# Kernel tuning notes

Measured on AMD Instinct MI355X. Metric: run time of the kernel, lower is better.

The kernel has to match this reference:

```python
import jax, jax.numpy as jnp
import numpy as np

D, L, C, CP, H, HD, QB, KB = 8, 2048, 128, 16, 4, 32, 32, 128
NQ = L // QB

def _ln(x, eps=1e-5):
    m = jnp.mean(x, axis=-1, keepdims=True)
    v = jnp.var(x, axis=-1, keepdims=True)
    return (x - m) * jax.lax.rsqrt(v + eps)

def _ada_ln(a, s, Wg, bg, Ws):
    # AF3 AdaLN: gated layernorm conditioned on s
    an = _ln(a); sn = _ln(s)
    return jax.nn.sigmoid(sn @ Wg + bg) * an + sn @ Ws

def setup_inputs() -> dict:
    key = jax.random.key(0)
    ks = jax.random.split(key, 32)
    p = lambda i, shape: jax.random.normal(ks[i], shape, dtype=jnp.float32) * 0.02
    inp = {}
    inp['A_I'] = jax.random.normal(ks[0], (D, L, C), dtype=jnp.float32)
    inp['S_I'] = jax.random.normal(ks[1], (D, L, C), dtype=jnp.float32)
    inp['Z_II'] = jax.random.normal(ks[2], (1, L, L, CP), dtype=jnp.float32)
    # static sliding-window indices: 128-key window centered on each 32-query block
    inp['indicesQ'] = jnp.arange(L, dtype=jnp.int64).reshape(NQ, QB)
    kraw = (jnp.arange(NQ) * QB - (KB - QB) // 2)[:, None] + jnp.arange(KB)[None, :]
    inp['indicesK'] = jnp.clip(kraw, 0, L - 1).astype(jnp.int64)
    inp['maskQ_float'] = jnp.zeros((NQ, QB), jnp.float32)
    inp['maskK_float'] = ((kraw < 0) | (kraw >= L)).astype(jnp.float32)
    # parameters
    inp['ada1_Wg'] = p(3, (C, C)); inp['ada1_bg'] = jnp.zeros((C,), jnp.float32); inp['ada1_Ws'] = p(4, (C, C))
    inp['Wq'] = p(5, (C, H * HD)); inp['bq'] = jnp.zeros((H * HD,), jnp.float32)
    inp['Wk'] = p(6, (C, H * HD)); inp['Wv'] = p(7, (C, H * HD))
    inp['ln0_g'] = jnp.ones((CP,), jnp.float32); inp['ln0_b'] = jnp.zeros((CP,), jnp.float32)
    inp['Wb'] = p(8, (CP, H))
    inp['Wg_attn'] = p(9, (C, H * HD))
    inp['Wa'] = p(10, (H * HD, C))
    inp['Wop'] = p(11, (C, C)); inp['bop'] = jnp.full((C,), -2.0, jnp.float32)
    inp['ada2_Wg'] = p(12, (C, C)); inp['ada2_bg'] = jnp.zeros((C,), jnp.float32); inp['ada2_Ws'] = p(13, (C, C))
    inp['W_sw'] = p(14, (C, 2 * C)); inp['W_lin'] = p(15, (C, 2 * C))
    inp['ct_Wg'] = p(16, (C, C)); inp['ct_bg'] = jnp.full((C,), -2.0, jnp.float32)
    inp['W_out2'] = p(17, (2 * C, C))
    return inp

def _forward(A_I, S_I, Z_II, indicesQ, indicesK, maskQ_float, maskK_float,
             ada1_Wg, ada1_bg, ada1_Ws, Wq, bq, Wk, Wv, ln0_g, ln0_b, Wb,
             Wg_attn, Wa, Wop, bop, ada2_Wg, ada2_bg, ada2_Ws, W_sw, W_lin,
             ct_Wg, ct_bg, W_out2):
    Dn, Lv = A_I.shape[0], A_I.shape[1]
    An = _ada_ln(A_I, S_I, ada1_Wg, ada1_bg, ada1_Ws)
    Q = (An @ Wq + bq).reshape(Dn, Lv, H, HD)
    K = (An @ Wk).reshape(Dn, Lv, H, HD)
    V = (An @ Wv).reshape(Dn, Lv, H, HD)
    B = ((_ln(Z_II) * ln0_g + ln0_b) @ Wb)[0]        # [L, L, H]
    G = jax.nn.sigmoid(An @ Wg_attn).reshape(Dn, Lv, H, HD)
    qs = Q[:, indicesQ]                              # [D, nq, qb, H, hd]
    ksub = K[:, indicesK]                            # [D, nq, kb, H, hd]
    vs = V[:, indicesK]
    attn = jnp.einsum('dnihc,dnjhc->dnijh', qs, ksub) / jnp.sqrt(jnp.float32(HD))
    bias = B[indicesQ[:, :, None], indicesK[:, None, :]]  # [nq, qb, kb, H]
    attn = attn + bias[None]
    mask = maskQ_float[None, :, :, None, None] + maskK_float[None, :, None, :, None]
    attn = attn - 1e9 * mask
    attn = jax.nn.softmax(attn, axis=-2)             # softmax over key window (j)
    af = jnp.einsum('dnijh,dnjhc->dnihc', attn, vs)
    af = af * (1.0 - maskQ_float)[None, :, :, None, None]
    af = af.reshape(Dn, -1, H, HD)[:, :Lv]
    af = (G * af).reshape(Dn, Lv, H * HD) @ Wa
    B_I = jax.nn.sigmoid(S_I @ Wop + bop) * af
    A = A_I + B_I
    an2 = _ada_ln(A, S_I, ada2_Wg, ada2_bg, ada2_Ws)
    b = jax.nn.silu(an2 @ W_sw) * (an2 @ W_lin)      # SwiGLU transition
    A = A + jax.nn.sigmoid(S_I @ ct_Wg + ct_bg) * (b @ W_out2)
    return A

def reference(A_I, S_I, Z_II, indicesQ, indicesK, maskQ_float, maskK_float,
              ada1_Wg, ada1_bg, ada1_Ws, Wq, bq, Wk, Wv, ln0_g, ln0_b, Wb,
              Wg_attn, Wa, Wop, bop, ada2_Wg, ada2_bg, ada2_Ws, W_sw, W_lin,
              ct_Wg, ct_bg, W_out2):
    return _forward(A_I, S_I, Z_II, indicesQ, indicesK, maskQ_float, maskK_float,
                    ada1_Wg, ada1_bg, ada1_Ws, Wq, bq, Wk, Wv, ln0_g, ln0_b, Wb,
                    Wg_attn, Wa, Wop, bop, ada2_Wg, ada2_bg, ada2_Ws, W_sw, W_lin,
                    ct_Wg, ct_bg, W_out2)
```

## Files before the change

kernel.cpp:

```cpp
#include <hip/hip_runtime.h>

#define DL 16384
#define LL 2048
#define NQB 64
#define QBS 32
#define KBS 128

typedef __attribute__((ext_vector_type(8))) short short8;
typedef __attribute__((ext_vector_type(4))) short short4v;
typedef __attribute__((ext_vector_type(4))) float f32x4;

__device__ __forceinline__ float sigmoidf_(float x) { return 1.f / (1.f + expf(-x)); }

__device__ __forceinline__ short f2bf(float f) {
    union { float f; unsigned u; } v; v.f = f;
    unsigned r = (v.u + 0x7FFFu + ((v.u >> 16) & 1u)) >> 16;
    return (short)r;
}
__device__ __forceinline__ float bf2f(short h) {
    union { unsigned u; float f; } v; v.u = ((unsigned)(unsigned short)h) << 16;
    return v.f;
}
__device__ __forceinline__ unsigned packbf16(short a, short b) {
    return ((unsigned)(unsigned short)a) | (((unsigned)(unsigned short)b) << 16);
}

#define AFRAG(buf, stride, r0, kk) (*(const short8*)&(buf)[(size_t)((r0) + cl) * (stride) + (kk) * 32 + kg * 8])
#define WFRAG(Wt, K, n0, kk) (*(const short8*)((Wt) + (size_t)((n0) + cl) * (K) + (kk) * 32 + kg * 8))
#define MFMA(acc, a, b) acc = __builtin_amdgcn_mfma_f32_16x16x32_bf16(a, b, acc, 0, 0, 0)

__global__ __launch_bounds__(256) void k_wtrans(
    const float* __restrict__ W0, const float* __restrict__ W1, const float* __restrict__ W2,
    const float* __restrict__ W3, const float* __restrict__ W4, const float* __restrict__ W5,
    const float* __restrict__ W6, const float* __restrict__ W7, const float* __restrict__ W8,
    const float* __restrict__ W9, const float* __restrict__ W10,
    const float* __restrict__ Wsw, const float* __restrict__ Wlin, const float* __restrict__ Wout2,
    short* __restrict__ wout)
{
    __shared__ float sW[128 * 128];
    const int b = blockIdx.x;
    const int tid = threadIdx.x;
    const float* srcs[14] = {W0,W1,W2,W3,W4,W5,W6,W7,W8,W9,W10,Wsw,Wlin,Wout2};
    const int sel[17]  = {0,1,2,3,4,5,6,7,8,9,10,11,11,12,12,13,13};
    const int soff[17] = {0,0,0,0,0,0,0,0,0,0,0, 0,128, 0,128, 0,16384};
    const int sN[17]   = {128,128,128,128,128,128,128,128,128,128,128, 256,256,256,256, 128,128};
    const int doff[17] = {0,16384,32768,49152,65536,81920,98304,114688,131072,147456,163840,
                          180224,196608, 212992,229376, 245760,245888};
    const int dK[17]   = {128,128,128,128,128,128,128,128,128,128,128, 128,128,128,128, 256,256};
    const float* src = srcs[sel[b]] + soff[b];
    const int srcN = sN[b];
    short* dst = wout + doff[b];
    const int dstK = dK[b];
    {
        const int r = tid >> 1, ch = (tid & 1) * 64;
        #pragma unroll
        for (int u = 0; u < 16; ++u) {
            float4 v = *(const float4*)(src + (size_t)r * srcN + ch + u * 4);
            *(float4*)&sW[r * 128 + ch + u * 4] = v;
        }
    }
    __syncthreads();
    {
        const int o = tid >> 1, kh = (tid & 1) * 64;
        #pragma unroll
        for (int u8 = 0; u8 < 8; ++u8) {
            short8 pk;
            #pragma unroll
            for (int e = 0; e < 8; ++e)
                pk[e] = f2bf(sW[(kh + u8 * 8 + e) * 128 + o]);
            *(short8*)(dst + (size_t)o * dstK + kh + u8 * 8) = pk;
        }
    }
}

__global__ __launch_bounds__(512) void k_main(
    const float* __restrict__ A_I, const float* __restrict__ S_I,
    const short* __restrict__ Wg1t, const short* __restrict__ Ws1t,
    const short* __restrict__ Wqt, const short* __restrict__ Wkt,
    const short* __restrict__ Wvt, const short* __restrict__ Wgat,
    const float* __restrict__ bg1, const float* __restrict__ bq,
    const float* __restrict__ Z, const float* __restrict__ g16, const float* __restrict__ b16,
    const float* __restrict__ Wb,
    short* __restrict__ Qo, short* __restrict__ Ko, short* __restrict__ Vo, short* __restrict__ Go,
    short* __restrict__ BBt)
{
    __shared__ short sAr[32 * 136];
    __shared__ short sSn[32 * 136];
    __shared__ short sAn[32 * 136];
    __shared__ float sMean[32], sRstd[32];
    __shared__ float sWb[64], sg[16], sb[16];
    __shared__ short sT[4 * 4 * 128];
    const int bid = blockIdx.x;
    const int tid = threadIdx.x;
    const int lane = tid & 63;

    if (bid >= 512) {
        const int bb = bid - 512;
        const int n = bb >> 3;
        const int io = (bb & 7) * 4;
        if (tid < 64) sWb[tid] = Wb[tid];
        if (tid < 16) { sg[tid] = g16[tid]; sb[tid] = b16[tid]; }
        __syncthreads();
        {
            int il = tid >> 7, j = tid & 127;
            int i = io + il;
            int kr = n * 32 - 48 + j;
            int kc = min(max(kr, 0), LL - 1);
            const float4* z4 = (const float4*)(Z + ((long)(n * 32 + i) * LL + kc) * 16);
            float zv[16];
            #pragma unroll
            for (int w = 0; w < 4; ++w) {
                float4 v = z4[w];
                zv[w * 4 + 0] = v.x; zv[w * 4 + 1] = v.y; zv[w * 4 + 2] = v.z; zv[w * 4 + 3] = v.w;
            }
            float sm = 0.f, sq = 0.f;
            #pragma unroll
            for (int cp = 0; cp < 16; ++cp) { sm += zv[cp]; sq = fmaf(zv[cp], zv[cp], sq); }
            float m = sm * (1.f / 16.f);
            float rs = rsqrtf(sq * (1.f / 16.f) - m * m + 1e-5f);
            float b0 = 0.f, b1 = 0.f, b2 = 0.f, b3 = 0.f;
            #pragma unroll
            for (int cp = 0; cp < 16; ++cp) {
                float zn = (zv[cp] - m) * rs * sg[cp] + sb[cp];
                b0 = fmaf(zn, sWb[cp * 4 + 0], b0);
                b1 = fmaf(zn, sWb[cp * 4 + 1], b1);
                b2 = fmaf(zn, sWb[cp * 4 + 2], b2);
                b3 = fmaf(zn, sWb[cp * 4 + 3], b3);
            }
            sT[(0 * 4 + il) * 128 + j] = f2bf(b0);
            sT[(1 * 4 + il) * 128 + j] = f2bf(b1);
            sT[(2 * 4 + il) * 128 + j] = f2bf(b2);
            sT[(3 * 4 + il) * 128 + j] = f2bf(b3);
        }
        __syncthreads();
        {
            int hh = tid >> 7, rem = tid & 127;
            int il = rem >> 5, jb = (rem & 31) * 4;
            short4v pk = *(const short4v*)&sT[(hh * 4 + il) * 128 + jb];
            *(short4v*)(BBt + (((size_t)n * 4 + hh) * 32 + io + il) * 128 + jb) = pk;
        }
        return;
    }

    const long t0 = (long)bid * 32;
    {
        const int row = tid >> 4, seg = tid & 15;
        const float* ap = A_I + (t0 + row) * 128 + seg * 8;
        const float* sp = S_I + (t0 + row) * 128 + seg * 8;
        float av[8], sv[8];
        #pragma unroll
        for (int u = 0; u < 2; ++u) {
            float4 a4 = ((const float4*)ap)[u];
            float4 s4 = ((const float4*)sp)[u];
            av[4*u] = a4.x; av[4*u+1] = a4.y; av[4*u+2] = a4.z; av[4*u+3] = a4.w;
            sv[4*u] = s4.x; sv[4*u+1] = s4.y; sv[4*u+2] = s4.z; sv[4*u+3] = s4.w;
        }
        float am = 0.f, aq = 0.f, sm = 0.f, sq = 0.f;
        #pragma unroll
        for (int u = 0; u < 8; ++u) {
            am += av[u]; aq = fmaf(av[u], av[u], aq);
            sm += sv[u]; sq = fmaf(sv[u], sv[u], sq);
        }
        am += __shfl_xor(am, 1); am += __shfl_xor(am, 2); am += __shfl_xor(am, 4); am += __shfl_xor(am, 8);
        aq += __shfl_xor(aq, 1); aq += __shfl_xor(aq, 2); aq += __shfl_xor(aq, 4); aq += __shfl_xor(aq, 8);
        sm += __shfl_xor(sm, 1); sm += __shfl_xor(sm, 2); sm += __shfl_xor(sm, 4); sm += __shfl_xor(sm, 8);
        sq += __shfl_xor(sq, 1); sq += __shfl_xor(sq, 2); sq += __shfl_xor(sq, 4); sq += __shfl_xor(sq, 8);
        float amean = am * (1.f / 128.f);
        float arstd = rsqrtf(aq * (1.f / 128.f) - amean * amean + 1e-5f);
        float smean = sm * (1.f / 128.f);
        float srstd = rsqrtf(sq * (1.f / 128.f) - smean * smean + 1e-5f);
        if ((tid & 15) == 0) { sMean[row] = amean; sRstd[row] = arstd; }
        short8 pa, ps;
        #pragma unroll
        for (int e = 0; e < 8; ++e) {
            pa[e] = f2bf(av[e]);
            ps[e] = f2bf((sv[e] - smean) * srstd);
        }
        *(short8*)&sAr[row * 136 + seg * 8] = pa;
        *(short8*)&sSn[row * 136 + seg * 8] = ps;
    }
    __syncthreads();
    const int w = tid >> 6;
    const int n0 = w * 16;
    const int cl = lane & 15, kg = lane >> 4;
    {
        short8 wg[4], wsf[4];
        #pragma unroll
        for (int kk = 0; kk < 4; ++kk) {
            wg[kk]  = WFRAG(Wg1t, 128, n0, kk);
            wsf[kk] = WFRAG(Ws1t, 128, n0, kk);
        }
        #pragma unroll
        for (int mt = 0; mt < 2; ++mt) {
            f32x4 ag = {0.f, 0.f, 0.f, 0.f}, as = {0.f, 0.f, 0.f, 0.f};
            #pragma unroll
            for (int kk = 0; kk < 4; ++kk) {
                short8 a = AFRAG(sSn, 136, mt * 16, kk);
                MFMA(ag, wg[kk], a);
                MFMA(as, wsf[kk], a);
            }
            const int tok = mt * 16 + cl;
            const int c0 = n0 + kg * 4;
            float4 bg4 = *(const float4*)&bg1[c0];
            float mean = sMean[tok], rstd = sRstd[tok];
            short4v ar4 = *(const short4v*)&sAr[tok * 136 + c0];
            short4v o;
            #pragma unroll
            for (int i = 0; i < 4; ++i) {
                float an = (bf2f(ar4[i]) - mean) * rstd;
                float An = sigmoidf_(ag[i] + ((const float*)&bg4)[i]) * an + as[i];
                o[i] = f2bf(An);
            }
            *(short4v*)&sAn[tok * 136 + c0] = o;
        }
    }
    __syncthreads();
    {
        const float SCL = 0.17677669529663687f;
        short8 af[2][4];
        #pragma unroll
        for (int mt = 0; mt < 2; ++mt)
            #pragma unroll
            for (int kk = 0; kk < 4; ++kk)
                af[mt][kk] = AFRAG(sAn, 136, mt * 16, kk);
        const int c0 = n0 + kg * 4;
        float4 bq4 = *(const float4*)&bq[c0];
        #pragma unroll
        for (int m = 0; m < 4; ++m) {
            const short* Wt = (m == 0) ? Wqt : (m == 1) ? Wkt : (m == 2) ? Wvt : Wgat;
            short8 wf[4];
            #pragma unroll
            for (int kk = 0; kk < 4; ++kk) wf[kk] = WFRAG(Wt, 128, n0, kk);
            #pragma unroll
            for (int mt = 0; mt < 2; ++mt) {
                f32x4 acc = {0.f, 0.f, 0.f, 0.f};
                #pragma unroll
                for (int kk = 0; kk < 4; ++kk) MFMA(acc, wf[kk], af[mt][kk]);
                long t = t0 + mt * 16 + cl;
                short4v o;
                if (m == 0) {
                    #pragma unroll
                    for (int i = 0; i < 4; ++i) o[i] = f2bf((acc[i] + ((const float*)&bq4)[i]) * SCL);
                    *(short4v*)(Qo + t * 128 + c0) = o;
                } else if (m == 1) {
                    #pragma unroll
                    for (int i = 0; i < 4; ++i) o[i] = f2bf(acc[i]);
                    *(short4v*)(Ko + t * 128 + c0) = o;
                } else if (m == 2) {
                    #pragma unroll
                    for (int i = 0; i < 4; ++i) o[i] = f2bf(acc[i]);
                    *(short4v*)(Vo + t * 128 + c0) = o;
                } else {
                    #pragma unroll
                    for (int i = 0; i < 4; ++i) o[i] = f2bf(sigmoidf_(acc[i]));
                    *(short4v*)(Go + t * 128 + c0) = o;
                }
            }
        }
    }
}

__global__ __launch_bounds__(512) void k_attn_postf(
    const short* __restrict__ Qg, const short* __restrict__ Kg, const short* __restrict__ Vg,
    const short* __restrict__ Gg, const short* __restrict__ BBt, const float* __restrict__ maskK,
    const float* __restrict__ S_I, const float* __restrict__ A_I,
    const short* __restrict__ Wat, const short* __restrict__ Wopt, const short* __restrict__ ctWgt,
    const short* __restrict__ Wg2t, const short* __restrict__ Ws2t,
    const short* __restrict__ Wswt, const short* __restrict__ Wlint, const short* __restrict__ Wout2t,
    const float* __restrict__ bop, const float* __restrict__ ctbg, const float* __restrict__ bg2,
    float* __restrict__ Out)
{
    __shared__ __align__(16) char smem[78336];
    short* sAF  = (short*)smem;
    short* vts  = (short*)(smem + 8704);
    short* Pl   = (short*)(smem + 43520);
    short* sS   = (short*)(smem + 8704);
    short* sSn  = (short*)(smem + 17408);
    float* sA   = (float*)(smem + 26112);
    float* sMean = (float*)(smem + 43008);
    float* sRstd = (float*)(smem + 43136);
    short* sAn2 = sAF;
    short* sB   = (short*)(smem + 8704);

    const int n = blockIdx.x, d = blockIdx.y;
    const int tid = threadIdx.x;
    const int lane = tid & 63;
    const long tb = (long)d * LL;
    const long t0 = tb + n * 32;
    const int kbase = n * 32 - 48;
    const int cl = lane & 15, kg = lane >> 4;
    const int w = tid >> 6;
    const int h = w >> 1, amt = w & 1;

    {
        const int unit = tid >> 1, half = tid & 1;
        const int hh = unit >> 6, j0 = (unit & 63) * 2;
        int kc0 = min(max(kbase + j0, 0), LL - 1);
        int kc1 = min(max(kbase + j0 + 1, 0), LL - 1);
        const short8* p0 = (const short8*)(Vg + (tb + kc0) * 128 + hh * 32 + half * 16);
        const short8* p1 = (const short8*)(Vg + (tb + kc1) * 128 + hh * 32 + half * 16);
        short8 e0 = p0[0], e1 = p0[1];
        short8 o0 = p1[0], o1 = p1[1];
        short* vh = vts + hh * 4352;
        #pragma unroll
        for (int e = 0; e < 8; ++e)
            *(unsigned*)&vh[(half * 16 + e) * 136 + j0] = packbf16(e0[e], o0[e]);
        #pragma unroll
        for (int e = 0; e < 8; ++e)
            *(unsigned*)&vh[(half * 16 + 8 + e) * 136 + j0] = packbf16(e1[e], o1[e]);
    }

    float sc[8][4];
    {
        short8 qf = *(const short8*)(Qg + (t0 + amt * 16 + cl) * 128 + h * 32 + kg * 8);
        #pragma unroll
        for (int nt = 0; nt < 8; ++nt) {
            int kc = min(max(kbase + nt * 16 + cl, 0), LL - 1);
            short8 kf = *(const short8*)(Kg + (tb + kc) * 128 + h * 32 + kg * 8);
            f32x4 s = {0.f, 0.f, 0.f, 0.f};
            MFMA(s, kf, qf);
            float4 mk4 = *(const float4*)(maskK + n * 128 + nt * 16 + kg * 4);
            short4v bfr = *(const short4v*)(BBt + (((size_t)n * 4 + h) * 32 + amt * 16 + cl) * 128 + nt * 16 + kg * 4);
            #pragma unroll
            for (int i = 0; i < 4; ++i)
                sc[nt][i] = s[i] + bf2f(bfr[i]) - ((const float*)&mk4)[i] * 1e9f;
        }
    }
    {
        float mx = sc[0][0];
        #pragma unroll
        for (int nt = 0; nt < 8; ++nt)
            #pragma unroll
            for (int i = 0; i < 4; ++i) mx = fmaxf(mx, sc[nt][i]);
        mx = fmaxf(mx, __shfl_xor(mx, 16));
        mx = fmaxf(mx, __shfl_xor(mx, 32));
        float sm = 0.f;
        #pragma unroll
        for (int nt = 0; nt < 8; ++nt)
            #pragma unroll
            for (int i = 0; i < 4; ++i) {
                float p = __expf(sc[nt][i] - mx);
                sc[nt][i] = p; sm += p;
            }
        sm += __shfl_xor(sm, 16);
        sm += __shfl_xor(sm, 32);
        float inv = 1.f / sm;
        short* PH = Pl + h * 4352;
        const int tok = amt * 16 + cl;
        #pragma unroll
        for (int nt = 0; nt < 8; ++nt) {
            short4v p4;
            #pragma unroll
            for (int i = 0; i < 4; ++i) p4[i] = f2bf(sc[nt][i] * inv);
            *(short4v*)&PH[tok * 136 + nt * 16 + kg * 4] = p4;
        }
    }

    const int prow = tid >> 4, pseg = tid & 15;
    float pav[8], psv[8];
    {
        const float* apI = A_I + (t0 + prow) * 128 + pseg * 8;
        const float* spI = S_I + (t0 + prow) * 128 + pseg * 8;
        #pragma unroll
        for (int u = 0; u < 2; ++u) {
            float4 a4 = ((const float4*)apI)[u];
            float4 s4 = ((const float4*)spI)[u];
            pav[4*u] = a4.x; pav[4*u+1] = a4.y; pav[4*u+2] = a4.z; pav[4*u+3] = a4.w;
            psv[4*u] = s4.x; psv[4*u+1] = s4.y; psv[4*u+2] = s4.z; psv[4*u+3] = s4.w;
        }
    }

    __syncthreads();
    {
        short* PH = Pl + h * 4352;
        short* vh = vts + h * 4352;
        const int tok = amt * 16 + cl;
        short8 pfr[4];
        #pragma unroll
        for (int kk = 0; kk < 4; ++kk)
            pfr[kk] = *(const short8*)&PH[tok * 136 + kk * 32 + kg * 8];
        #pragma unroll
        for (int ct = 0; ct < 2; ++ct) {
            f32x4 acc = {0.f, 0.f, 0.f, 0.f};
            #pragma unroll
            for (int kk = 0; kk < 4; ++kk) {
                short8 a = *(const short8*)&vh[(ct * 16 + cl) * 136 + kk * 32 + kg * 8];
                MFMA(acc, a, pfr[kk]);
            }
            const int c0 = h * 32 + ct * 16 + kg * 4;
            short4v g4 = *(const short4v*)(Gg + (t0 + tok) * 128 + c0);
            short4v o4;
            #pragma unroll
            for (int i = 0; i < 4; ++i) o4[i] = f2bf(bf2f(g4[i]) * acc[i]);
            *(short4v*)&sAF[tok * 136 + c0] = o4;
        }
    }
    __syncthreads();

    {
        #pragma unroll
        for (int u = 0; u < 2; ++u)
            *(float4*)&sA[prow * 132 + pseg * 8 + u * 4] = *(const float4*)&pav[u * 4];
        float sm = 0.f, sq = 0.f;
        #pragma unroll
        for (int u = 0; u < 8; ++u) { sm += psv[u]; sq = fmaf(psv[u], psv[u], sq); }
        sm += __shfl_xor(sm, 1); sm += __shfl_xor(sm, 2); sm += __shfl_xor(sm, 4); sm += __shfl_xor(sm, 8);
        sq += __shfl_xor(sq, 1); sq += __shfl_xor(sq, 2); sq += __shfl_xor(sq, 4); sq += __shfl_xor(sq, 8);
        float smean = sm * (1.f / 128.f);
        float srstd = rsqrtf(sq * (1.f / 128.f) - smean * smean + 1e-5f);
        short8 pr, pn;
        #pragma unroll
        for (int e = 0; e < 8; ++e) {
            float s = psv[e];
            pr[e] = f2bf(s);
            pn[e] = f2bf((s - smean) * srstd);
        }
        *(short8*)&sS [prow * 136 + pseg * 8] = pr;
        *(short8*)&sSn[prow * 136 + pseg * 8] = pn;
    }
    __syncthreads();
    const int n0 = w * 16;
    const int c0 = n0 + kg * 4;
    float g2s[8];

    {
        short8 wA[4], wO[4], wG[4];
        #pragma unroll
        for (int kk = 0; kk < 4; ++kk) {
            wA[kk] = WFRAG(Wat, 128, n0, kk);
            wO[kk] = WFRAG(Wopt, 128, n0, kk);
            wG[kk] = WFRAG(ctWgt, 128, n0, kk);
        }
        float4 bop4 = *(const float4*)&bop[c0];
        float4 ct4  = *(const float4*)&ctbg[c0];
        #pragma unroll
        for (int rt = 0; rt < 2; ++rt) {
            f32x4 aA = {0.f,0.f,0.f,0.f}, aO = {0.f,0.f,0.f,0.f}, aG = {0.f,0.f,0.f,0.f};
            #pragma unroll
            for (int kk = 0; kk < 4; ++kk) {
                short8 af = AFRAG(sAF, 136, rt * 16, kk);
                short8 sf = AFRAG(sS, 136, rt * 16, kk);
                MFMA(aA, wA[kk], af);
                MFMA(aO, wO[kk], sf);
                MFMA(aG, wG[kk], sf);
            }
            const int tok = rt * 16 + cl;
            float4 Av = *(const float4*)&sA[tok * 132 + c0];
            float4 outv;
            #pragma unroll
            for (int i = 0; i < 4; ++i) {
                ((float*)&outv)[i] = ((const float*)&Av)[i]
                    + sigmoidf_(aO[i] + ((const float*)&bop4)[i]) * aA[i];
                g2s[rt * 4 + i] = sigmoidf_(aG[i] + ((const float*)&ct4)[i]);
            }
            *(float4*)&sA[tok * 132 + c0] = outv;
        }
    }
    __syncthreads();
    {
        float m = 0.f, q = 0.f;
        #pragma unroll
        for (int u = 0; u < 2; ++u) {
            float4 v = *(const float4*)&sA[prow * 132 + pseg * 8 + u * 4];
            m += v.x + v.y + v.z + v.w;
            q = fmaf(v.x, v.x, q); q = fmaf(v.y, v.y, q);
            q = fmaf(v.z, v.z, q); q = fmaf(v.w, v.w, q);
        }
        m += __shfl_xor(m, 1); m += __shfl_xor(m, 2); m += __shfl_xor(m, 4); m += __shfl_xor(m, 8);
        q += __shfl_xor(q, 1); q += __shfl_xor(q, 2); q += __shfl_xor(q, 4); q += __shfl_xor(q, 8);
        float mean = m * (1.f / 128.f);
        float rstd = rsqrtf(q * (1.f / 128.f) - mean * mean + 1e-5f);
        if ((tid & 15) == 0) { sMean[prow] = mean; sRstd[prow] = rstd; }
    }
    __syncthreads();
    {
        short8 wg2[4], ws2[4];
        #pragma unroll
        for (int kk = 0; kk < 4; ++kk) {
            wg2[kk] = WFRAG(Wg2t, 128, n0, kk);
            ws2[kk] = WFRAG(Ws2t, 128, n0, kk);
        }
        float4 bg24 = *(const float4*)&bg2[c0];
        #pragma unroll
        for (int rt = 0; rt < 2; ++rt) {
            f32x4 ag = {0.f,0.f,0.f,0.f}, as = {0.f,0.f,0.f,0.f};
            #pragma unroll
            for (int kk = 0; kk < 4; ++kk) {
                short8 a = AFRAG(sSn, 136, rt * 16, kk);
                MFMA(ag, wg2[kk], a);
                MFMA(as, ws2[kk], a);
            }
            const int tok = rt * 16 + cl;
            float mean = sMean[tok], rstd = sRstd[tok];
            float4 Av = *(const float4*)&sA[tok * 132 + c0];
            short4v o;
            #pragma unroll
            for (int i = 0; i < 4; ++i) {
                float lnA = (((const float*)&Av)[i] - mean) * rstd;
                o[i] = f2bf(sigmoidf_(ag[i] + ((const float*)&bg24)[i]) * lnA + as[i]);
            }
            *(short4v*)&sAn2[tok * 136 + c0] = o;
        }
    }
    __syncthreads();
    {
        short8 a2f[2][4];
        #pragma unroll
        for (int rt = 0; rt < 2; ++rt)
            #pragma unroll
            for (int kk = 0; kk < 4; ++kk)
                a2f[rt][kk] = AFRAG(sAn2, 136, rt * 16, kk);
        #pragma unroll
        for (int j = 0; j < 2; ++j) {
            const int n0b = w * 32 + j * 16;
            short8 ww[4], wl[4];
            #pragma unroll
            for (int kk = 0; kk < 4; ++kk) {
                ww[kk] = WFRAG(Wswt, 128, n0b, kk);
                wl[kk] = WFRAG(Wlint, 128, n0b, kk);
            }
            #pragma unroll
            for (int rt = 0; rt < 2; ++rt) {
                f32x4 aw = {0.f,0.f,0.f,0.f}, al = {0.f,0.f,0.f,0.f};
                #pragma unroll
                for (int kk = 0; kk < 4; ++kk) {
                    MFMA(aw, ww[kk], a2f[rt][kk]);
                    MFMA(al, wl[kk], a2f[rt][kk]);
                }
                const int tok = rt * 16 + cl;
                short4v o;
                #pragma unroll
                for (int i = 0; i < 4; ++i) {
                    float x = aw[i];
                    o[i] = f2bf((x / (1.f + expf(-x))) * al[i]);
                }
                *(short4v*)&sB[tok * 264 + n0b + kg * 4] = o;
            }
        }
    }
    __syncthreads();
    {
        short8 wo[8];
        #pragma unroll
        for (int kk = 0; kk < 8; ++kk) wo[kk] = WFRAG(Wout2t, 256, n0, kk);
        #pragma unroll
        for (int rt = 0; rt < 2; ++rt) {
            f32x4 acc = {0.f,0.f,0.f,0.f};
            #pragma unroll
            for (int kk = 0; kk < 8; ++kk) {
                short8 a = AFRAG(sB, 264, rt * 16, kk);
                MFMA(acc, wo[kk], a);
            }
            const int tok = rt * 16 + cl;
            float4 Av = *(const float4*)&sA[tok * 132 + c0];
            float4 outv;
            #pragma unroll
            for (int i = 0; i < 4; ++i)
                ((float*)&outv)[i] = ((const float*)&Av)[i] + g2s[rt * 4 + i] * acc[i];
            *(float4*)(Out + (t0 + tok) * 128 + c0) = outv;
        }
    }
}

extern "C" void kernel_launch(void* const* d_in, const int* in_sizes, int n_in,
                              void* d_out, int out_size, void* d_ws, size_t ws_size,
                              hipStream_t stream)
{
    const float* A_I  = (const float*)d_in[0];
    const float* S_I  = (const float*)d_in[1];
    const float* Z    = (const float*)d_in[2];
    const float* maskK = (const float*)d_in[6];
    const float* a1Wg = (const float*)d_in[7];
    const float* a1bg = (const float*)d_in[8];
    const float* a1Ws = (const float*)d_in[9];
    const float* Wq   = (const float*)d_in[10];
    const float* bq   = (const float*)d_in[11];
    const float* Wk   = (const float*)d_in[12];
    const float* Wv   = (const float*)d_in[13];
    const float* ln0g = (const float*)d_in[14];
    const float* ln0b = (const float*)d_in[15];
    const float* Wb   = (const float*)d_in[16];
    const float* Wga  = (const float*)d_in[17];
    const float* Wa   = (const float*)d_in[18];
    const float* Wop  = (const float*)d_in[19];
    const float* bop  = (const float*)d_in[20];
    const float* a2Wg = (const float*)d_in[21];
    const float* a2bg = (const float*)d_in[22];
    const float* a2Ws = (const float*)d_in[23];
    const float* Wsw  = (const float*)d_in[24];
    const float* Wlin = (const float*)d_in[25];
    const float* ctWg = (const float*)d_in[26];
    const float* ctbg = (const float*)d_in[27];
    const float* Wout2 = (const float*)d_in[28];
    float* out = (float*)d_out;

    const size_t NTC = (size_t)DL * 128;
    short* Qb = (short*)d_ws;
    short* Kb = Qb + NTC;
    short* Vb = Kb + NTC;
    short* Gb = Vb + NTC;
    short* BBt = Gb + NTC;
    short* wbt = BBt + (size_t)NQB * 4 * 32 * 128;

    short* Wg1t = wbt + 0 * 16384;
    short* Ws1t = wbt + 1 * 16384;
    short* Wqt  = wbt + 2 * 16384;
    short* Wkt  = wbt + 3 * 16384;
    short* Wvt  = wbt + 4 * 16384;
    short* Wgat = wbt + 5 * 16384;
    short* Wat  = wbt + 6 * 16384;
    short* Wopt = wbt + 7 * 16384;
    short* ctWgt = wbt + 8 * 16384;
    short* Wg2t = wbt + 9 * 16384;
    short* Ws2t = wbt + 10 * 16384;
    short* Wswt = wbt + 180224;
    short* Wlint = wbt + 212992;
    short* Wout2t = wbt + 245760;

    k_wtrans<<<17, 256, 0, stream>>>(a1Wg, a1Ws, Wq, Wk, Wv, Wga, Wa, Wop, ctWg,
                                     a2Wg, a2Ws, Wsw, Wlin, Wout2, wbt);
    k_main<<<1024, 512, 0, stream>>>(A_I, S_I, Wg1t, Ws1t, Wqt, Wkt, Wvt, Wgat,
                                     a1bg, bq, Z, ln0g, ln0b, Wb,
                                     Qb, Kb, Vb, Gb, BBt);
    k_attn_postf<<<dim3(NQB, 8), 512, 0, stream>>>(Qb, Kb, Vb, Gb, BBt, maskK,
                                                   S_I, A_I,
                                                   Wat, Wopt, ctWgt, Wg2t, Ws2t,
                                                   Wswt, Wlint, Wout2t,
                                                   bop, ctbg, a2bg, out);
}
```

Baseline: 68.67 us.

## Move downstream weight transposes into main kernel and reorder attention grid

The weight-transpose kernel now converts only the six weights k_main needs. The eleven transposes used only by the attention/post kernel become 11 extra blocks appended to k_main, so they run alongside the main work instead of serialising before it. k_main's static shared arrays are merged into one 64KB buffer reused by each block role, which may affect occupancy. The attention grid is flattened to 1D with d as the fastest index, and the gate load is hoisted ahead of the barrier to hide its latency.

```diff
diff --git a/kernel.cpp b/kernel.cpp
--- a/kernel.cpp
+++ b/kernel.cpp
@@ -32,30 +32,19 @@
 __global__ __launch_bounds__(256) void k_wtrans(
     const float* __restrict__ W0, const float* __restrict__ W1, const float* __restrict__ W2,
     const float* __restrict__ W3, const float* __restrict__ W4, const float* __restrict__ W5,
-    const float* __restrict__ W6, const float* __restrict__ W7, const float* __restrict__ W8,
-    const float* __restrict__ W9, const float* __restrict__ W10,
-    const float* __restrict__ Wsw, const float* __restrict__ Wlin, const float* __restrict__ Wout2,
     short* __restrict__ wout)
 {
     __shared__ float sW[128 * 128];
     const int b = blockIdx.x;
     const int tid = threadIdx.x;
-    const float* srcs[14] = {W0,W1,W2,W3,W4,W5,W6,W7,W8,W9,W10,Wsw,Wlin,Wout2};
-    const int sel[17]  = {0,1,2,3,4,5,6,7,8,9,10,11,11,12,12,13,13};
-    const int soff[17] = {0,0,0,0,0,0,0,0,0,0,0, 0,128, 0,128, 0,16384};
-    const int sN[17]   = {128,128,128,128,128,128,128,128,128,128,128, 256,256,256,256, 128,128};
-    const int doff[17] = {0,16384,32768,49152,65536,81920,98304,114688,131072,147456,163840,
-                          180224,196608, 212992,229376, 245760,245888};
-    const int dK[17]   = {128,128,128,128,128,128,128,128,128,128,128, 128,128,128,128, 256,256};
-    const float* src = srcs[sel[b]] + soff[b];
-    const int srcN = sN[b];
-    short* dst = wout + doff[b];
-    const int dstK = dK[b];
+    const float* srcs[6] = {W0,W1,W2,W3,W4,W5};
+    const float* src = srcs[b];
+    short* dst = wout + b * 16384;
     {
         const int r = tid >> 1, ch = (tid & 1) * 64;
         #pragma unroll
         for (int u = 0; u < 16; ++u) {
-            float4 v = *(const float4*)(src + (size_t)r * srcN + ch + u * 4);
+            float4 v = *(const float4*)(src + (size_t)r * 128 + ch + u * 4);
             *(float4*)&sW[r * 128 + ch + u * 4] = v;
         }
     }
@@ -68,7 +57,7 @@
             #pragma unroll
             for (int e = 0; e < 8; ++e)
                 pk[e] = f2bf(sW[(kh + u8 * 8 + e) * 128 + o]);
-            *(short8*)(dst + (size_t)o * dstK + kh + u8 * 8) = pk;
+            *(short8*)(dst + (size_t)o * 128 + kh + u8 * 8) = pk;
         }
     }
 }
@@ -81,20 +70,59 @@
     const float* __restrict__ bg1, const float* __restrict__ bq,
     const float* __restrict__ Z, const float* __restrict__ g16, const float* __restrict__ b16,
     const float* __restrict__ Wb,
+    const float* __restrict__ Wa, const float* __restrict__ Wop, const float* __restrict__ ctWg,
+    const float* __restrict__ a2Wg, const float* __restrict__ a2Ws,
+    const float* __restrict__ Wsw, const float* __restrict__ Wlin, const float* __restrict__ Wout2,
     short* __restrict__ Qo, short* __restrict__ Ko, short* __restrict__ Vo, short* __restrict__ Go,
-    short* __restrict__ BBt)
+    short* __restrict__ BBt, short* __restrict__ wbt)
 {
-    __shared__ short sAr[32 * 136];
-    __shared__ short sSn[32 * 136];
-    __shared__ short sAn[32 * 136];
-    __shared__ float sMean[32], sRstd[32];
-    __shared__ float sWb[64], sg[16], sb[16];
-    __shared__ short sT[4 * 4 * 128];
+    __shared__ __align__(16) char smem[65536];
     const int bid = blockIdx.x;
     const int tid = threadIdx.x;
     const int lane = tid & 63;
 
+    if (bid >= 1024) {
+        float* sW = (float*)smem;
+        const int b = bid - 1024;
+        const float* srcs[8] = {Wa,Wop,ctWg,a2Wg,a2Ws,Wsw,Wlin,Wout2};
+        const int sel[11]  = {0,1,2,3,4,5,5,6,6,7,7};
+        const int soff[11] = {0,0,0,0,0, 0,128, 0,128, 0,16384};
+        const int sN[11]   = {128,128,128,128,128, 256,256,256,256, 128,128};
+        const int doff[11] = {98304,114688,131072,147456,163840,
+                              180224,196608, 212992,229376, 245760,245888};
+        const int dK[11]   = {128,128,128,128,128, 128,128,128,128, 256,256};
+        const float* src = srcs[sel[b]] + soff[b];
+        const int srcN = sN[b];
+        short* dst = wbt + doff[b];
+        const int dstK = dK[b];
+        {
+            const int r = tid >> 2, ch = (tid & 3) * 32;
+            #pragma unroll
+            for (int u = 0; u < 8; ++u) {
+                float4 v = *(const float4*)(src + (size_t)r * srcN + ch + u * 4);
+                *(float4*)&sW[r * 128 + ch + u * 4] = v;
+            }
+        }
+        __syncthreads();
+        {
+            const int o = tid >> 2, kh = (tid & 3) * 32;
+            #pragma unroll
+            for (int u8 = 0; u8 < 4; ++u8) {
+                short8 pk;
+                #pragma unroll
+                for (int e = 0; e < 8; ++e)
+                    pk[e] = f2bf(sW[(kh + u8 * 8 + e) * 128 + o]);
+                *(short8*)(dst + (size_t)o * dstK + kh + u8 * 8) = pk;
+            }
+        }
+        return;
+    }
+
     if (bid >= 512) {
+        float* sWb = (float*)smem;
+        float* sg  = (float*)(smem + 256);
+        float* sb  = (float*)(smem + 320);
+        short* sT  = (short*)(smem + 384);
         const int bb = bid - 512;
         const int n = bb >> 3;
         const int io = (bb & 7) * 4;
@@ -142,6 +170,11 @@
         return;
     }
 
+    short* sAr = (short*)smem;
+    short* sSn = (short*)(smem + 8704);
+    short* sAn = (short*)(smem + 17408);
+    float* sMean = (float*)(smem + 26112);
+    float* sRstd = (float*)(smem + 26240);
     const long t0 = (long)bid * 32;
     {
         const int row = tid >> 4, seg = tid & 15;
@@ -282,7 +315,8 @@
     short* sAn2 = sAF;
     short* sB   = (short*)(smem + 8704);
 
-    const int n = blockIdx.x, d = blockIdx.y;
+    const int p = blockIdx.x;
+    const int n = p >> 3, d = p & 7;
     const int tid = threadIdx.x;
     const int lane = tid & 63;
     const long tb = (long)d * LL;
@@ -339,8 +373,8 @@
         for (int nt = 0; nt < 8; ++nt)
             #pragma unroll
             for (int i = 0; i < 4; ++i) {
-                float p = __expf(sc[nt][i] - mx);
-                sc[nt][i] = p; sm += p;
+                float pe = __expf(sc[nt][i] - mx);
+                sc[nt][i] = pe; sm += pe;
             }
         sm += __shfl_xor(sm, 16);
         sm += __shfl_xor(sm, 32);
@@ -369,6 +403,13 @@
             psv[4*u] = s4.x; psv[4*u+1] = s4.y; psv[4*u+2] = s4.z; psv[4*u+3] = s4.w;
         }
     }
+    short4v g4h[2];
+    {
+        const int tok = amt * 16 + cl;
+        #pragma unroll
+        for (int ct = 0; ct < 2; ++ct)
+            g4h[ct] = *(const short4v*)(Gg + (t0 + tok) * 128 + h * 32 + ct * 16 + kg * 4);
+    }
 
     __syncthreads();
     {
@@ -388,10 +429,9 @@
                 MFMA(acc, a, pfr[kk]);
             }
             const int c0 = h * 32 + ct * 16 + kg * 4;
-            short4v g4 = *(const short4v*)(Gg + (t0 + tok) * 128 + c0);
             short4v o4;
             #pragma unroll
-            for (int i = 0; i < 4; ++i) o4[i] = f2bf(bf2f(g4[i]) * acc[i]);
+            for (int i = 0; i < 4; ++i) o4[i] = f2bf(bf2f(g4h[ct][i]) * acc[i]);
             *(short4v*)&sAF[tok * 136 + c0] = o4;
         }
     }
@@ -617,14 +657,14 @@
     short* Wlint = wbt + 212992;
     short* Wout2t = wbt + 245760;
 
-    k_wtrans<<<17, 256, 0, stream>>>(a1Wg, a1Ws, Wq, Wk, Wv, Wga, Wa, Wop, ctWg,
-                                     a2Wg, a2Ws, Wsw, Wlin, Wout2, wbt);
-    k_main<<<1024, 512, 0, stream>>>(A_I, S_I, Wg1t, Ws1t, Wqt, Wkt, Wvt, Wgat,
+    k_wtrans<<<6, 256, 0, stream>>>(a1Wg, a1Ws, Wq, Wk, Wv, Wga, wbt);
+    k_main<<<1035, 512, 0, stream>>>(A_I, S_I, Wg1t, Ws1t, Wqt, Wkt, Wvt, Wgat,
                                      a1bg, bq, Z, ln0g, ln0b, Wb,
-                                     Qb, Kb, Vb, Gb, BBt);
-    k_attn_postf<<<dim3(NQB, 8), 512, 0, stream>>>(Qb, Kb, Vb, Gb, BBt, maskK,
-                                                   S_I, A_I,
-                                                   Wat, Wopt, ctWgt, Wg2t, Ws2t,
-                                                   Wswt, Wlint, Wout2t,
-                                                   bop, ctbg, a2bg, out);
+                                     Wa, Wop, ctWg, a2Wg, a2Ws, Wsw, Wlin, Wout2,
+                                     Qb, Kb, Vb, Gb, BBt, wbt);
+    k_attn_postf<<<512, 512, 0, stream>>>(Qb, Kb, Vb, Gb, BBt, maskK,
+                                          S_I, A_I,
+                                          Wat, Wopt, ctWgt, Wg2t, Ws2t,
+                                          Wswt, Wlint, Wout2t,
+                                          bop, ctbg, a2bg, out);
 }
```

Result: slower. 73.16 us (+6.5%).
